# Kernel tuning notes

Measured on AMD Instinct MI355X. Metric: run time of the kernel, lower is better.

The kernel has to match this reference:

```python
import jax, jax.numpy as jnp
import numpy as np

B, L, D, H = 2, 2048, 1024, 16
DK = D // H
DFF = 4 * D
EPS = 1e-5  # torch LayerNorm default


def setup_inputs() -> dict:
    key = jax.random.key(0)
    ks = jax.random.split(key, 12)
    w = lambda k, shp: (jax.random.normal(k, shp, jnp.float32) * 0.02)
    return {
        "x": jax.random.normal(ks[0], (B, L, D), jnp.float32),
        "y": jax.random.normal(ks[1], (B, L, D), jnp.float32),
        "Wq": w(ks[2], (D, D)), "bq": jnp.zeros((D,), jnp.float32),
        "Wk": w(ks[3], (D, D)), "bk": jnp.zeros((D,), jnp.float32),
        "Wv": w(ks[4], (D, D)), "bv": jnp.zeros((D,), jnp.float32),
        "Wo": w(ks[5], (D, D)), "bo": jnp.zeros((D,), jnp.float32),
        "W1": w(ks[6], (D, DFF)), "b1": jnp.zeros((DFF,), jnp.float32),
        "W2": w(ks[7], (DFF, D)), "b2": jnp.zeros((D,), jnp.float32),
        "ln1_w": jnp.ones((L, D), jnp.float32), "ln1_b": jnp.zeros((L, D), jnp.float32),
        "ln2_w": jnp.ones((L, D), jnp.float32), "ln2_b": jnp.zeros((L, D), jnp.float32),
    }


def _layernorm2d(t, w, b):
    # nn.LayerNorm(normalized_shape=[L, D]): normalize jointly over last two dims
    mu = jnp.mean(t, axis=(-2, -1), keepdims=True)
    var = jnp.mean((t - mu) ** 2, axis=(-2, -1), keepdims=True)
    return (t - mu) * jax.lax.rsqrt(var + EPS) * w + b


def _attention(q_in, kv_in, Wq, bq, Wk, bk, Wv, bv, Wo, bo):
    split = lambda t: t.reshape(B, L, H, DK).transpose(0, 2, 1, 3)  # [B,H,L,DK]
    q = split(q_in @ Wq + bq)
    k = split(kv_in @ Wk + bk)
    v = split(kv_in @ Wv + bv)
    scores = jnp.einsum("bhqd,bhkd->bhqk", q, k) / (DK ** 0.5)
    # NOTE: original applies torch.tril to SCORES (zeroes upper triangle,
    # NOT -inf), so future positions still contribute exp(0)=1 in softmax.
    scores = jnp.tril(scores)
    p_attn = jax.nn.softmax(scores, axis=-1)
    out = jnp.einsum("bhqk,bhkd->bhqd", p_attn, v)
    out = out.transpose(0, 2, 1, 3).reshape(B, L, D)
    return out @ Wo + bo


def reference(x, y, Wq, bq, Wk, bk, Wv, bv, Wo, bo, W1, b1, W2, b2,
              ln1_w, ln1_b, ln2_w, ln2_b):
    # sublayer 0: pre-norm y, attention(query=x, key=value=norm(y)), residual
    y1 = y + _attention(x, _layernorm2d(y, ln1_w, ln1_b),
                        Wq, bq, Wk, bk, Wv, bv, Wo, bo)
    # sublayer 1: pre-norm, FFN (dropout inactive in eval), residual
    h = jax.nn.relu(_layernorm2d(y1, ln2_w, ln2_b) @ W1 + b1)
    return y1 + h @ W2 + b2
```

## Files before the change

### kernel.cpp

```cpp
#include <hip/hip_runtime.h>
#include <math.h>

#define B 2
#define L 2048
#define D 1024
#define H 16
#define DK 64
#define DFF 4096
#define EPS 1e-5f

typedef short short8 __attribute__((ext_vector_type(8)));
typedef short short4v __attribute__((ext_vector_type(4)));
typedef float float4v __attribute__((ext_vector_type(4)));
typedef unsigned int u32;

__device__ inline short f2bf(float f) {
    unsigned u = __builtin_bit_cast(unsigned, f);
    u += 0x7fffu + ((u >> 16) & 1u);
    return (short)(u >> 16);
}

__device__ inline float bf2f(short s) {
    unsigned u = ((unsigned)(unsigned short)s) << 16;
    return __builtin_bit_cast(float, u);
}

#define GLOAD_LDS16(gp, lp)                                                  \
    __builtin_amdgcn_global_load_lds(                                        \
        (const __attribute__((address_space(1))) u32*)(const void*)(gp),     \
        (__attribute__((address_space(3))) u32*)(void*)(lp), 16, 0, 0)

__device__ inline void xcd_remap(int& bx, int& by) {
    const int nbx = gridDim.x, nby = gridDim.y;
    const int orig = blockIdx.x + nbx * blockIdx.y;
    const int k = orig & 7, j = orig >> 3;
    const int nyc = nby >> 3;
    bx = j % nbx;
    by = k * nyc + j / nbx;
}


__global__ __launch_bounds__(256) void red_partial(const float* __restrict__ X,
                                                   float* __restrict__ part) {
    int b = blockIdx.y;
    const float4* p = (const float4*)(X + (size_t)b * L * D);
    float s = 0.f, ss = 0.f;
    for (int idx = blockIdx.x * 256 + threadIdx.x; idx < L * D / 4; idx += 256 * 256) {
        float4 v = p[idx];
        s += v.x + v.y + v.z + v.w;
        ss += v.x * v.x + v.y * v.y + v.z * v.z + v.w * v.w;
    }
    __shared__ float sh0[256], sh1[256];
    sh0[threadIdx.x] = s; sh1[threadIdx.x] = ss;
    __syncthreads();
    for (int o = 128; o; o >>= 1) {
        if (threadIdx.x < o) {
            sh0[threadIdx.x] += sh0[threadIdx.x + o];
            sh1[threadIdx.x] += sh1[threadIdx.x + o];
        }
        __syncthreads();
    }
    if (threadIdx.x == 0) {
        part[(b * 256 + blockIdx.x) * 2 + 0] = sh0[0];
        part[(b * 256 + blockIdx.x) * 2 + 1] = sh1[0];
    }
}

__global__ __launch_bounds__(256) void red_final(const float* __restrict__ part,
                                                 float* __restrict__ stats) {
    int b = blockIdx.x;
    float s = part[(b * 256 + threadIdx.x) * 2 + 0];
    float ss = part[(b * 256 + threadIdx.x) * 2 + 1];
    __shared__ float sh0[256], sh1[256];
    sh0[threadIdx.x] = s; sh1[threadIdx.x] = ss;
    __syncthreads();
    for (int o = 128; o; o >>= 1) {
        if (threadIdx.x < o) {
            sh0[threadIdx.x] += sh0[threadIdx.x + o];
            sh1[threadIdx.x] += sh1[threadIdx.x + o];
        }
        __syncthreads();
    }
    if (threadIdx.x == 0) {
        const float invN = 1.f / (float)(L * D);
        float mu = sh0[0] * invN;
        float var = sh1[0] * invN - mu * mu;
        stats[b * 2 + 0] = mu;
        stats[b * 2 + 1] = rsqrtf(var + EPS);
    }
}

__global__ __launch_bounds__(256) void ln_apply_bf(const float* __restrict__ X,
                                                   const float* __restrict__ W,
                                                   const float* __restrict__ Bb,
                                                   const float* __restrict__ stats,
                                                   short* __restrict__ Yn) {
    int b = blockIdx.y;
    float mu = stats[b * 2 + 0];
    float rstd = stats[b * 2 + 1];
    size_t e = (size_t)(blockIdx.x * 256 + threadIdx.x) * 4;
    const float4 xv = *(const float4*)(X + (size_t)b * L * D + e);
    const float4 wv = *(const float4*)(W + e);
    const float4 bv = *(const float4*)(Bb + e);
    short4v o;
    o[0] = f2bf((xv.x - mu) * rstd * wv.x + bv.x);
    o[1] = f2bf((xv.y - mu) * rstd * wv.y + bv.y);
    o[2] = f2bf((xv.z - mu) * rstd * wv.z + bv.z);
    o[3] = f2bf((xv.w - mu) * rstd * wv.w + bv.w);
    *(short4v*)(Yn + (size_t)b * L * D + e) = o;
}

__global__ __launch_bounds__(256) void convert_bf(const float* __restrict__ X,
                                                  short* __restrict__ Y) {
    size_t e = (size_t)(blockIdx.x * 256 + threadIdx.x) * 4;
    const float4 v = *(const float4*)(X + e);
    short4v o = {f2bf(v.x), f2bf(v.y), f2bf(v.z), f2bf(v.w)};
    *(short4v*)(Y + e) = o;
}

__global__ __launch_bounds__(256) void wt_transpose(const float* __restrict__ W,
                                                    short* __restrict__ WT,
                                                    int K, int N) {
    __shared__ short tile[32][33];
    const int t = threadIdx.x;
    const int tx = t & 31, ty = t >> 5;
    const int k0 = blockIdx.y * 32, n0 = blockIdx.x * 32;
#pragma unroll
    for (int i = 0; i < 4; ++i) {
        const int k = ty + i * 8;
        tile[k][tx] = f2bf(W[(size_t)(k0 + k) * N + n0 + tx]);
    }
    __syncthreads();
#pragma unroll
    for (int i = 0; i < 4; ++i) {
        const int n = ty + i * 8;
        WT[(size_t)(n0 + n) * K + k0 + tx] = tile[tx][n];
    }
}


__device__ __forceinline__ void cv128_body(const short* __restrict__ A,
                                           const short* __restrict__ BT,
                                           const float* __restrict__ bias,
                                           const float* __restrict__ Res,
                                           void* __restrict__ Cout,
                                           int N, int Kloop, int lda, int flags,
                                           int m0, int n0,
                                           short* __restrict__ AsB,
                                           short* __restrict__ BsB) {
    const int t = threadIdx.x;
    const int wave = t >> 6, lane = t & 63;
    const int m16 = lane & 15, q4 = lane >> 4;
    const int wm = (wave >> 1) * 64, wn = (wave & 1) * 64;
    const int xorm = m16 & 7;
    const int BUFE = 128 * 64;

    float4v acc[4][4];
#pragma unroll
    for (int i = 0; i < 4; ++i)
#pragma unroll
        for (int j = 0; j < 4; ++j) acc[i][j] = (float4v){0.f, 0.f, 0.f, 0.f};

    auto stage = [&](int buf, int k0) {
        short* AsBuf = AsB + buf * BUFE;
        short* BsBuf = BsB + buf * BUFE;
#pragma unroll
        for (int p = 0; p < 4; ++p) {
            const int s = p * 256 + t;
            const int row = s >> 3;
            const int col = ((s & 7) ^ (row & 7)) * 8;
            GLOAD_LDS16(A + (size_t)(m0 + row) * lda + k0 + col,
                        AsBuf + (p * 256 + wave * 64) * 8);
        }
#pragma unroll
        for (int p = 0; p < 4; ++p) {
            const int s = p * 256 + t;
            const int row = s >> 3;
            const int col = ((s & 7) ^ (row & 7)) * 8;
            GLOAD_LDS16(BT + (size_t)(n0 + row) * lda + k0 + col,
                        BsBuf + (p * 256 + wave * 64) * 8);
        }
    };

    auto compute = [&](int buf) {
        const short* AsBuf = AsB + buf * BUFE;
        const short* BsBuf = BsB + buf * BUFE;
#pragma unroll
        for (int kk = 0; kk < 2; ++kk) {
            const int slot = ((kk * 4 + q4) ^ xorm) * 8;
            short8 af[4], bf[4];
#pragma unroll
            for (int mi = 0; mi < 4; ++mi)
                af[mi] = *(const short8*)&AsBuf[(wm + mi * 16 + m16) * 64 + slot];
#pragma unroll
            for (int ni = 0; ni < 4; ++ni)
                bf[ni] = *(const short8*)&BsBuf[(wn + ni * 16 + m16) * 64 + slot];
#pragma unroll
            for (int mi = 0; mi < 4; ++mi)
#pragma unroll
                for (int ni = 0; ni < 4; ++ni)
                    acc[mi][ni] = __builtin_amdgcn_mfma_f32_16x16x32_bf16(
                        af[mi], bf[ni], acc[mi][ni], 0, 0, 0);
        }
    };

    const int nt = Kloop >> 6;
    stage(0, 0);
    for (int ti = 0; ti < nt; ++ti) {
        const int cur = ti & 1;
        if (ti + 1 < nt) {
            stage(cur ^ 1, (ti + 1) << 6);
            asm volatile("s_waitcnt vmcnt(8)" ::: "memory");
        } else {
            asm volatile("s_waitcnt vmcnt(0)" ::: "memory");
        }
        __builtin_amdgcn_s_barrier();
        __builtin_amdgcn_sched_barrier(0);
        compute(cur);
        __builtin_amdgcn_s_barrier();
    }

#pragma unroll
    for (int mi = 0; mi < 4; ++mi)
#pragma unroll
        for (int ni = 0; ni < 4; ++ni) {
            const int col = n0 + wn + ni * 16 + m16;
            const float bb = bias ? bias[col] : 0.f;
#pragma unroll
            for (int r = 0; r < 4; ++r) {
                const int row = m0 + wm + mi * 16 + q4 * 4 + r;
                float v = acc[mi][ni][r] + bb;
                if (Res) v += Res[(size_t)row * N + col];
                if (flags & 1) v = fmaxf(v, 0.f);
                if (flags & 2)
                    ((short*)Cout)[(size_t)row * N + col] = f2bf(v);
                else
                    ((float*)Cout)[(size_t)row * N + col] = v;
            }
        }
}

__global__ __launch_bounds__(256) void gemm_cv128(const short* __restrict__ A,
                                                  const short* __restrict__ BT,
                                                  const float* __restrict__ bias,
                                                  const float* __restrict__ Res,
                                                  void* __restrict__ Cout,
                                                  int M, int N, int K, int flags) {
    __shared__ short As[2][128 * 64];
    __shared__ short Bs[2][128 * 64];
    int bx, by;
    xcd_remap(bx, by);
    cv128_body(A, BT, bias, Res, Cout, N, K, K, flags, by * 128, bx * 128,
               &As[0][0], &Bs[0][0]);
}

__global__ __launch_bounds__(256) void gemm_qkv(const short* __restrict__ xb,
                                                const short* __restrict__ WqT,
                                                const float* __restrict__ bq,
                                                short* __restrict__ qb,
                                                const short* __restrict__ ynb,
                                                const short* __restrict__ WkvT,
                                                const float* __restrict__ bkv,
                                                short* __restrict__ kvb) {
    __shared__ short As[2][128 * 64];
    __shared__ short Bs[2][128 * 64];
    const int id = blockIdx.x;
    const int k = id & 7, j = id >> 3;
    const int lin = k * 96 + j;
    if (lin < 256) {
        const int bx = lin & 7, by = lin >> 3;
        cv128_body(xb, WqT, bq, nullptr, qb, 1024, 1024, 1024, 2,
                   by * 128, bx * 128, &As[0][0], &Bs[0][0]);
    } else {
        const int l2 = lin - 256;
        const int bx = l2 & 15, by = l2 >> 4;
        cv128_body(ynb, WkvT, bkv, nullptr, kvb, 2048, 1024, 1024, 2,
                   by * 128, bx * 128, &As[0][0], &Bs[0][0]);
    }
}

__global__ __launch_bounds__(256) void gemm_cv128_sk(const short* __restrict__ A,
                                                     const short* __restrict__ BT,
                                                     float* __restrict__ part,
                                                     int M, int N, int K) {
    __shared__ short As[2][128 * 64];
    __shared__ short Bs[2][128 * 64];
    const int id = blockIdx.x;
    const int k = id & 7, j = id >> 3;
    const int lin = k * 64 + j;
    const int ks = lin >> 8;
    const int rem = lin & 255;
    const int by = rem & 31, bx = (rem >> 5) & 7;
    const int Kc = K >> 1;
    cv128_body(A + ks * Kc, BT + ks * Kc, nullptr, nullptr,
               part + (size_t)ks * M * N, N, Kc, K, 0,
               by * 128, bx * 128, &As[0][0], &Bs[0][0]);
}

__global__ __launch_bounds__(256) void sk_reduce(const float* __restrict__ part,
                                                 const float* __restrict__ bias,
                                                 const float* __restrict__ Res,
                                                 float* __restrict__ out,
                                                 int MN, int N) {
    const size_t e = (size_t)(blockIdx.x * 256 + threadIdx.x) * 4;
    const float4 p0 = *(const float4*)(part + e);
    const float4 p1 = *(const float4*)(part + (size_t)MN + e);
    const float4 rv = *(const float4*)(Res + e);
    const float4 bv = *(const float4*)(bias + (e & (size_t)(N - 1)));
    float4 o;
    o.x = p0.x + p1.x + rv.x + bv.x;
    o.y = p0.y + p1.y + rv.y + bv.y;
    o.z = p0.z + p1.z + rv.z + bv.z;
    o.w = p0.w + p1.w + rv.w + bv.w;
    *(float4*)(out + e) = o;
}

__global__ __launch_bounds__(512) void gemm_cv256(const short* __restrict__ A,
                                                  const short* __restrict__ BT,
                                                  const float* __restrict__ bias,
                                                  const float* __restrict__ Res,
                                                  void* __restrict__ Cout,
                                                  int M, int N, int K, int flags) {
    __shared__ short As[2][256 * 64];
    __shared__ short Bs[2][256 * 64];
    const int t = threadIdx.x;
    const int wave = t >> 6, lane = t & 63;
    const int m16 = lane & 15, q4 = lane >> 4;
    int bx, by;
    xcd_remap(bx, by);
    const int m0 = by * 256, n0 = bx * 256;
    const int wm = (wave >> 2) * 128, wn = (wave & 3) * 64;
    const int xorm = m16 & 7;

    float4v acc[8][4];
#pragma unroll
    for (int i = 0; i < 8; ++i)
#pragma unroll
        for (int j = 0; j < 4; ++j) acc[i][j] = (float4v){0.f, 0.f, 0.f, 0.f};

    auto stage = [&](int buf, int k0) {
#pragma unroll
        for (int p = 0; p < 4; ++p) {
            const int s = p * 512 + t;
            const int row = s >> 3;
            const int col = ((s & 7) ^ (row & 7)) * 8;
            short* lds = &As[buf][(p * 512 + wave * 64) * 8];
            GLOAD_LDS16(A + (size_t)(m0 + row) * K + k0 + col, lds);
        }
#pragma unroll
        for (int p = 0; p < 4; ++p) {
            const int s = p * 512 + t;
            const int row = s >> 3;
            const int col = ((s & 7) ^ (row & 7)) * 8;
            short* lds = &Bs[buf][(p * 512 + wave * 64) * 8];
            GLOAD_LDS16(BT + (size_t)(n0 + row) * K + k0 + col, lds);
        }
    };

    auto compute = [&](int buf) {
#pragma unroll
        for (int kk = 0; kk < 2; ++kk) {
            const int slot = ((kk * 4 + q4) ^ xorm) * 8;
            short8 af[8], bf[4];
#pragma unroll
            for (int mi = 0; mi < 8; ++mi)
                af[mi] = *(const short8*)&As[buf][(wm + mi * 16 + m16) * 64 + slot];
#pragma unroll
            for (int ni = 0; ni < 4; ++ni)
                bf[ni] = *(const short8*)&Bs[buf][(wn + ni * 16 + m16) * 64 + slot];
#pragma unroll
            for (int mi = 0; mi < 8; ++mi)
#pragma unroll
                for (int ni = 0; ni < 4; ++ni)
                    acc[mi][ni] = __builtin_amdgcn_mfma_f32_16x16x32_bf16(
                        af[mi], bf[ni], acc[mi][ni], 0, 0, 0);
        }
    };

    const int nt = K >> 6;
    stage(0, 0);
    for (int ti = 0; ti < nt; ++ti) {
        const int cur = ti & 1;
        if (ti + 1 < nt) {
            stage(cur ^ 1, (ti + 1) << 6);
            asm volatile("s_waitcnt vmcnt(8)" ::: "memory");
        } else {
            asm volatile("s_waitcnt vmcnt(0)" ::: "memory");
        }
        __builtin_amdgcn_s_barrier();
        __builtin_amdgcn_sched_barrier(0);
        compute(cur);
        __builtin_amdgcn_s_barrier();
    }

#pragma unroll
    for (int mi = 0; mi < 8; ++mi)
#pragma unroll
        for (int ni = 0; ni < 4; ++ni) {
            const int col = n0 + wn + ni * 16 + m16;
            const float bb = bias[col];
#pragma unroll
            for (int r = 0; r < 4; ++r) {
                const int row = m0 + wm + mi * 16 + q4 * 4 + r;
                float v = acc[mi][ni][r] + bb;
                if (Res) v += Res[(size_t)row * N + col];
                if (flags & 1) v = fmaxf(v, 0.f);
                if (flags & 2)
                    ((short*)Cout)[(size_t)row * N + col] = f2bf(v);
                else
                    ((float*)Cout)[(size_t)row * N + col] = v;
            }
        }
}


#define ASTR 72
#define SKV (2 * D)

__global__ __launch_bounds__(256) void v_tilesum(const short* __restrict__ KVg,
                                                 float* __restrict__ Vtile) {
    const int bh = blockIdx.x >> 5;
    const int kt = blockIdx.x & 31;
    const int b = bh >> 4, h = bh & (H - 1);
    const size_t baseV = (size_t)b * L * SKV + (size_t)h * DK + D;
    const int d = threadIdx.x & 63, g = threadIdx.x >> 6;
    float s = 0.f;
    for (int j = g * 16; j < g * 16 + 16; ++j)
        s += bf2f(KVg[baseV + (size_t)(kt * 64 + j) * SKV + d]);
    __shared__ float sh[4][64];
    sh[g][d] = s;
    __syncthreads();
    if (threadIdx.x < 64)
        Vtile[((size_t)bh * 32 + kt) * 64 + d] = sh[0][d] + sh[1][d] + sh[2][d] + sh[3][d];
}

__global__ __launch_bounds__(64) void v_suffix(const float* __restrict__ Vtile,
                                               float* __restrict__ Vsuf) {
    const int bh = blockIdx.x;
    const int d = threadIdx.x;
    float s = 0.f;
    Vsuf[((size_t)bh * 33 + 32) * 64 + d] = 0.f;
    for (int kt = 31; kt >= 0; --kt) {
        s += Vtile[((size_t)bh * 32 + kt) * 64 + d];
        Vsuf[((size_t)bh * 33 + kt) * 64 + d] = s;
    }
}


__global__ __launch_bounds__(256) void v_transpose(const short* __restrict__ KVg,
                                                   short* __restrict__ VT) {
    __shared__ short tile[64 * ASTR];
    const int t = threadIdx.x;
    const int bh = blockIdx.x >> 5;
    const int jt = blockIdx.x & 31;
    const int b = bh >> 4, h = bh & (H - 1);
    const size_t baseV = (size_t)b * L * SKV + (size_t)h * DK + D;
    const int j0 = jt * 64;
    const int sj = t >> 3, sd8 = (t & 7) * 8, sm = t & 7;
#pragma unroll
    for (int rep = 0; rep < 2; ++rep) {
        const int j = rep * 32 + sj;
        const short8 vv = *(const short8*)(KVg + baseV + (size_t)(j0 + j) * SKV + sd8);
        const int jsw = ((((j >> 3) ^ sm) << 3) | (j & 7));
#pragma unroll
        for (int i = 0; i < 8; ++i) tile[(sd8 + i) * ASTR + jsw] = vv[i];
    }
    __syncthreads();
#pragma unroll
    for (int rep = 0; rep < 2; ++rep) {
        const int s = rep * 256 + t;
        const int d = s >> 3, c = s & 7;
        const short8 vv = *(const short8*)&tile[d * ASTR + ((c ^ (d >> 3)) << 3)];
        *(short8*)(VT + ((size_t)bh * DK + d) * L + j0 + c * 8) = vv;
    }
}


__global__ __launch_bounds__(256) void attn_mfma(const short* __restrict__ Qg,
                                                 const short* __restrict__ KVg,
                                                 const short* __restrict__ VTg,
                                                 const float* __restrict__ Vsuf,
                                                 short* __restrict__ O) {
    __shared__ alignas(16) short Kb[2][64 * 64];
    __shared__ alignas(16) short Vt[2][64 * 64];
    __shared__ alignas(16) short Pb[64 * ASTR];

    const int t = threadIdx.x;
    const int wave = t >> 6;
    const int lane = t & 63;
    const int m16 = lane & 15;
    const int q4 = lane >> 4;

    const int u = blockIdx.x & 15;
    const int bh = blockIdx.x >> 4;
    const int h = bh & (H - 1);
    const int b = bh >> 4;
    const size_t baseQ = (size_t)b * L * D + (size_t)h * DK;
    const size_t baseK = (size_t)b * L * SKV + (size_t)h * DK;
    const size_t baseVT = (size_t)bh * DK * L;

    const int irow = wave * 16 + m16;
    const int ig = irow >> 3;
    const int xorm = m16 & 7;

    auto stage = [&](int buf, int kt0) {
#pragma unroll
        for (int rep = 0; rep < 2; ++rep) {
            const int s = rep * 256 + t;
            const int j = s >> 3;
            const int c = (s & 7) ^ (j & 7);
            GLOAD_LDS16(KVg + baseK + (size_t)(kt0 + j) * SKV + c * 8,
                        &Kb[buf][(rep * 256 + wave * 64) * 8]);
        }
#pragma unroll
        for (int rep = 0; rep < 2; ++rep) {
            const int s = rep * 256 + t;
            const int d = s >> 3;
            const int c = (s & 7) ^ (d & 7);
            GLOAD_LDS16(VTg + baseVT + (size_t)d * L + kt0 + c * 8,
                        &Vt[buf][(rep * 256 + wave * 64) * 8]);
        }
    };

#pragma unroll
    for (int pq = 0; pq < 2; ++pq) {
        const int qt = pq ? (31 - u) : u;
        const int q0 = qt * 64;
        const int rowA = q0 + wave * 16 + m16;

        short8 qf[2];
#pragma unroll
        for (int kc = 0; kc < 2; ++kc)
            qf[kc] = *(const short8*)(Qg + baseQ + (size_t)rowA * D + kc * 32 + q4 * 8);

        float lsum = 0.f;
        float4v acc[4];
#pragma unroll
        for (int f = 0; f < 4; ++f) acc[f] = (float4v){0.f, 0.f, 0.f, 0.f};

        stage(0, 0);
        for (int kt = 0; kt <= qt; ++kt) {
            const int cur = kt & 1;
            if (kt < qt) {
                stage(cur ^ 1, (kt + 1) * 64);
                asm volatile("s_waitcnt vmcnt(4)" ::: "memory");
            } else {
                asm volatile("s_waitcnt vmcnt(0)" ::: "memory");
            }
            __builtin_amdgcn_s_barrier();
            __builtin_amdgcn_sched_barrier(0);

            const short* KbC = &Kb[cur][0];
            const short* VtC = &Vt[cur][0];
            const bool diag = (kt == qt);

#pragma unroll
            for (int f = 0; f < 4; ++f) {
                const int krow = f * 16 + m16;
                const short8 kf0 = *(const short8*)&KbC[krow * 64 + ((q4 ^ xorm) << 3)];
                const short8 kf1 = *(const short8*)&KbC[krow * 64 + (((4 + q4) ^ xorm) << 3)];
                float4v sv = {0.f, 0.f, 0.f, 0.f};
                sv = __builtin_amdgcn_mfma_f32_16x16x32_bf16(kf0, qf[0], sv, 0, 0, 0);
                sv = __builtin_amdgcn_mfma_f32_16x16x32_bf16(kf1, qf[1], sv, 0, 0, 0);

                float pv[4];
                if (diag) {
#pragma unroll
                    for (int r = 0; r < 4; ++r) {
                        const int jl = f * 16 + q4 * 4 + r;
                        pv[r] = (jl <= irow) ? __expf(sv[r] * 0.125f) : 1.0f;
                    }
                } else {
#pragma unroll
                    for (int r = 0; r < 4; ++r) pv[r] = __expf(sv[r] * 0.125f);
                }
                lsum += pv[0] + pv[1] + pv[2] + pv[3];

                short4v s4;
                s4[0] = f2bf(pv[0]); s4[1] = f2bf(pv[1]);
                s4[2] = f2bf(pv[2]); s4[3] = f2bf(pv[3]);
                const int jb = f * 2 + (q4 >> 1);
                *(short4v*)&Pb[irow * ASTR + (((jb ^ ig) << 3) | ((q4 & 1) << 2))] = s4;
            }

#pragma unroll
            for (int kc = 0; kc < 2; ++kc) {
                const short8 pf = *(const short8*)&Pb[irow * ASTR + (((kc * 4 + q4) ^ ig) << 3)];
#pragma unroll
                for (int f = 0; f < 4; ++f) {
                    const int d = f * 16 + m16;
                    const short8 vf = *(const short8*)&VtC[d * 64 + (((kc * 4 + q4) ^ xorm) << 3)];
                    acc[f] = __builtin_amdgcn_mfma_f32_16x16x32_bf16(pf, vf, acc[f], 0, 0, 0);
                }
            }
            __builtin_amdgcn_s_barrier();
        }

        float s = lsum;
        s += __shfl_xor(s, 16);
        s += __shfl_xor(s, 32);
        s += (float)(L - (qt + 1) * 64);
        const float inv = 1.0f / s;
        float invr[4];
#pragma unroll
        for (int r = 0; r < 4; ++r) invr[r] = __shfl(inv, q4 * 4 + r);

        const float* vs = Vsuf + ((size_t)bh * 33 + qt + 1) * 64;
#pragma unroll
        for (int f = 0; f < 4; ++f) {
            const float vadd = vs[f * 16 + m16];
#pragma unroll
            for (int r = 0; r < 4; ++r) {
                const int i = q0 + wave * 16 + q4 * 4 + r;
                O[baseQ + (size_t)i * D + f * 16 + m16] = f2bf((acc[f][r] + vadd) * invr[r]);
            }
        }
    }
}


extern "C" void kernel_launch(void* const* d_in, const int* in_sizes, int n_in,
                              void* d_out, int out_size, void* d_ws, size_t ws_size,
                              hipStream_t stream) {
    const float* x    = (const float*)d_in[0];
    const float* y    = (const float*)d_in[1];
    const float* Wq   = (const float*)d_in[2];
    const float* bq   = (const float*)d_in[3];
    const float* Wk   = (const float*)d_in[4];
    const float* bk   = (const float*)d_in[5];
    const float* Wv   = (const float*)d_in[6];
    const float* bv   = (const float*)d_in[7];
    const float* Wo   = (const float*)d_in[8];
    const float* bo   = (const float*)d_in[9];
    const float* W1   = (const float*)d_in[10];
    const float* b1   = (const float*)d_in[11];
    const float* W2   = (const float*)d_in[12];
    const float* b2   = (const float*)d_in[13];
    const float* ln1w = (const float*)d_in[14];
    const float* ln1b = (const float*)d_in[15];
    const float* ln2w = (const float*)d_in[16];
    const float* ln2b = (const float*)d_in[17];
    float* out = (float*)d_out;

    const size_t F = (size_t)B * L * D;
    char* p = (char*)d_ws;
    short* xb    = (short*)p; p += F * 2;
    short* ynb   = (short*)p; p += F * 2;
    short* qb    = (short*)p; p += F * 2;
    short* kvb   = (short*)p; p += 2 * F * 2;
    short* aob   = (short*)p; p += F * 2;
    short* y1nb  = (short*)p; p += F * 2;
    short* hb    = (short*)p; p += (size_t)B * L * DFF * 2;
    float* y1    = (float*)p; p += F * 4;
    short* WqT   = (short*)p; p += (size_t)D * D * 2;
    short* WkvT  = (short*)p; p += (size_t)D * 2 * D * 2;
    short* WoT   = (short*)p; p += (size_t)D * D * 2;
    short* W1T   = (short*)p; p += (size_t)D * DFF * 2;
    short* W2T   = (short*)p; p += (size_t)D * DFF * 2;
    float* biaskv= (float*)p; p += 2 * D * 4;
    float* vtile = (float*)p; p += (size_t)B * H * 32 * DK * 4;
    float* vsuf  = (float*)p; p += (size_t)B * H * 33 * DK * 4;
    float* part  = (float*)p; p += B * 256 * 2 * 4;
    float* stats = (float*)p;

    short* vtb = hb;
    float* skpart = (float*)qb;

    const int M = B * L;

    wt_transpose<<<dim3(D / 32, D / 32), 256, 0, stream>>>(Wq, WqT, D, D);
    wt_transpose<<<dim3(D / 32, D / 32), 256, 0, stream>>>(Wk, WkvT, D, D);
    wt_transpose<<<dim3(D / 32, D / 32), 256, 0, stream>>>(Wv, WkvT + (size_t)D * D, D, D);
    wt_transpose<<<dim3(D / 32, D / 32), 256, 0, stream>>>(Wo, WoT, D, D);
    wt_transpose<<<dim3(DFF / 32, D / 32), 256, 0, stream>>>(W1, W1T, D, DFF);
    wt_transpose<<<dim3(D / 32, DFF / 32), 256, 0, stream>>>(W2, W2T, DFF, D);
    hipMemcpyAsync(biaskv,     bk, D * sizeof(float), hipMemcpyDeviceToDevice, stream);
    hipMemcpyAsync(biaskv + D, bv, D * sizeof(float), hipMemcpyDeviceToDevice, stream);

    convert_bf<<<dim3(F / 1024), 256, 0, stream>>>(x, xb);

    red_partial<<<dim3(256, B), 256, 0, stream>>>(y, part);
    red_final<<<dim3(B), 256, 0, stream>>>(part, stats);
    ln_apply_bf<<<dim3(L * D / 1024, B), 256, 0, stream>>>(y, ln1w, ln1b, stats, ynb);

    gemm_qkv<<<dim3(768), 256, 0, stream>>>(xb, WqT, bq, qb, ynb, WkvT, biaskv, kvb);

    v_transpose<<<dim3(B * H * 32), 256, 0, stream>>>(kvb, vtb);
    v_tilesum<<<dim3(B * H * 32), 256, 0, stream>>>(kvb, vtile);
    v_suffix<<<dim3(B * H), 64, 0, stream>>>(vtile, vsuf);

    attn_mfma<<<dim3(B * H * 16), 256, 0, stream>>>(qb, kvb, vtb, vsuf, aob);

    gemm_cv128<<<dim3(D / 128, M / 128), 256, 0, stream>>>(aob, WoT, bo, y, y1, M, D, D, 0);

    red_partial<<<dim3(256, B), 256, 0, stream>>>(y1, part);
    red_final<<<dim3(B), 256, 0, stream>>>(part, stats);
    ln_apply_bf<<<dim3(L * D / 1024, B), 256, 0, stream>>>(y1, ln2w, ln2b, stats, y1nb);

    gemm_cv256<<<dim3(DFF / 256, M / 256), 512, 0, stream>>>(y1nb, W1T, b1, nullptr, hb, M, DFF, D, 3);

    gemm_cv128_sk<<<dim3(512), 256, 0, stream>>>(hb, W2T, skpart, M, D, DFF);
    sk_reduce<<<dim3(M * D / 1024), 256, 0, stream>>>(skpart, b2, y1, out, M * D, D);
}
```

Baseline: 429.3 us.

## Merge weight transposes, fuse V tilesum, triple-buffer attention, split-K Wo GEMM

Folds the six weight-transpose launches into one kernel and fuses the V tile-sum into the V transpose kernel, which cuts launch count and an extra read of V. The attention kernel moves to a three-stage K/V buffer, raises wave priority around the MFMA section, uses exp2f with a folded scale, and packs the bf16 conversion with v_cvt_pk_bf16_f32. The Wo projection switches from a 128x128 tiled GEMM to the split-K GEMM plus a reduction kernel. The extra buffer stage uses more LDS, which can lower occupancy, and split-K adds an extra pass over partial sums.

Result: faster. 410.6 us (-4.3%).

```diff
diff --git a/kernel.cpp b/kernel.cpp
--- a/kernel.cpp
+++ b/kernel.cpp
@@ -118,13 +118,28 @@
     *(short4v*)(Y + e) = o;
 }
 
-__global__ __launch_bounds__(256) void wt_transpose(const float* __restrict__ W,
-                                                    short* __restrict__ WT,
-                                                    int K, int N) {
+__global__ __launch_bounds__(256) void wt_transpose_all(
+        const float* __restrict__ Wq, const float* __restrict__ Wk,
+        const float* __restrict__ Wv, const float* __restrict__ Wo,
+        const float* __restrict__ W1, const float* __restrict__ W2,
+        short* __restrict__ WqT, short* __restrict__ WkvT,
+        short* __restrict__ WoT, short* __restrict__ W1T,
+        short* __restrict__ W2T) {
+    const int id = blockIdx.x;
+    const float* W; short* WT; int K, N, rel;
+    if (id < 1024)      { W = Wq; WT = WqT;                    K = 1024; N = 1024; rel = id; }
+    else if (id < 2048) { W = Wk; WT = WkvT;                   K = 1024; N = 1024; rel = id - 1024; }
+    else if (id < 3072) { W = Wv; WT = WkvT + (size_t)D * D;   K = 1024; N = 1024; rel = id - 2048; }
+    else if (id < 4096) { W = Wo; WT = WoT;                    K = 1024; N = 1024; rel = id - 3072; }
+    else if (id < 8192) { W = W1; WT = W1T;                    K = 1024; N = 4096; rel = id - 4096; }
+    else                { W = W2; WT = W2T;                    K = 4096; N = 1024; rel = id - 8192; }
+    const int lb = (N == 4096) ? 7 : 5;
+    const int bx = rel & ((1 << lb) - 1), by = rel >> lb;
+
     __shared__ short tile[32][33];
     const int t = threadIdx.x;
     const int tx = t & 31, ty = t >> 5;
-    const int k0 = blockIdx.y * 32, n0 = blockIdx.x * 32;
+    const int k0 = by * 32, n0 = bx * 32;
 #pragma unroll
     for (int i = 0; i < 4; ++i) {
         const int k = ty + i * 8;
@@ -238,20 +253,6 @@
                     ((float*)Cout)[(size_t)row * N + col] = v;
             }
         }
-}
-
-__global__ __launch_bounds__(256) void gemm_cv128(const short* __restrict__ A,
-                                                  const short* __restrict__ BT,
-                                                  const float* __restrict__ bias,
-                                                  const float* __restrict__ Res,
-                                                  void* __restrict__ Cout,
-                                                  int M, int N, int K, int flags) {
-    __shared__ short As[2][128 * 64];
-    __shared__ short Bs[2][128 * 64];
-    int bx, by;
-    xcd_remap(bx, by);
-    cv128_body(A, BT, bias, Res, Cout, N, K, K, flags, by * 128, bx * 128,
-               &As[0][0], &Bs[0][0]);
 }
 
 __global__ __launch_bounds__(256) void gemm_qkv(const short* __restrict__ xb,
@@ -417,21 +418,45 @@
 #define ASTR 72
 #define SKV (2 * D)
 
-__global__ __launch_bounds__(256) void v_tilesum(const short* __restrict__ KVg,
-                                                 float* __restrict__ Vtile) {
+__global__ __launch_bounds__(256) void v_transpose(const short* __restrict__ KVg,
+                                                   short* __restrict__ VT,
+                                                   float* __restrict__ Vtile) {
+    __shared__ short tile[64 * ASTR];
+    __shared__ float sh[4][64];
+    const int t = threadIdx.x;
     const int bh = blockIdx.x >> 5;
-    const int kt = blockIdx.x & 31;
+    const int jt = blockIdx.x & 31;
     const int b = bh >> 4, h = bh & (H - 1);
     const size_t baseV = (size_t)b * L * SKV + (size_t)h * DK + D;
-    const int d = threadIdx.x & 63, g = threadIdx.x >> 6;
-    float s = 0.f;
-    for (int j = g * 16; j < g * 16 + 16; ++j)
-        s += bf2f(KVg[baseV + (size_t)(kt * 64 + j) * SKV + d]);
-    __shared__ float sh[4][64];
-    sh[g][d] = s;
+    const int j0 = jt * 64;
+    const int sj = t >> 3, sd8 = (t & 7) * 8, sm = t & 7;
+#pragma unroll
+    for (int rep = 0; rep < 2; ++rep) {
+        const int j = rep * 32 + sj;
+        const short8 vv = *(const short8*)(KVg + baseV + (size_t)(j0 + j) * SKV + sd8);
+        const int jsw = ((((j >> 3) ^ sm) << 3) | (j & 7));
+#pragma unroll
+        for (int i = 0; i < 8; ++i) tile[(sd8 + i) * ASTR + jsw] = vv[i];
+    }
     __syncthreads();
-    if (threadIdx.x < 64)
-        Vtile[((size_t)bh * 32 + kt) * 64 + d] = sh[0][d] + sh[1][d] + sh[2][d] + sh[3][d];
+#pragma unroll
+    for (int rep = 0; rep < 2; ++rep) {
+        const int s = rep * 256 + t;
+        const int d = s >> 3, c = s & 7;
+        const short8 vv = *(const short8*)&tile[d * ASTR + ((c ^ (d >> 3)) << 3)];
+        *(short8*)(VT + ((size_t)bh * DK + d) * L + j0 + c * 8) = vv;
+    }
+    {
+        const int d = t & 63, g = t >> 6;
+        float s = 0.f;
+#pragma unroll
+        for (int c = 0; c < 16; ++c) s += bf2f(tile[d * ASTR + g * 16 + c]);
+        sh[g][d] = s;
+        __syncthreads();
+        if (t < 64)
+            Vtile[((size_t)bh * 32 + jt) * 64 + t] =
+                sh[0][t] + sh[1][t] + sh[2][t] + sh[3][t];
+    }
 }
 
 __global__ __launch_bounds__(64) void v_suffix(const float* __restrict__ Vtile,
@@ -447,42 +472,13 @@
 }
 
 
-__global__ __launch_bounds__(256) void v_transpose(const short* __restrict__ KVg,
-                                                   short* __restrict__ VT) {
-    __shared__ short tile[64 * ASTR];
-    const int t = threadIdx.x;
-    const int bh = blockIdx.x >> 5;
-    const int jt = blockIdx.x & 31;
-    const int b = bh >> 4, h = bh & (H - 1);
-    const size_t baseV = (size_t)b * L * SKV + (size_t)h * DK + D;
-    const int j0 = jt * 64;
-    const int sj = t >> 3, sd8 = (t & 7) * 8, sm = t & 7;
-#pragma unroll
-    for (int rep = 0; rep < 2; ++rep) {
-        const int j = rep * 32 + sj;
-        const short8 vv = *(const short8*)(KVg + baseV + (size_t)(j0 + j) * SKV + sd8);
-        const int jsw = ((((j >> 3) ^ sm) << 3) | (j & 7));
-#pragma unroll
-        for (int i = 0; i < 8; ++i) tile[(sd8 + i) * ASTR + jsw] = vv[i];
-    }
-    __syncthreads();
-#pragma unroll
-    for (int rep = 0; rep < 2; ++rep) {
-        const int s = rep * 256 + t;
-        const int d = s >> 3, c = s & 7;
-        const short8 vv = *(const short8*)&tile[d * ASTR + ((c ^ (d >> 3)) << 3)];
-        *(short8*)(VT + ((size_t)bh * DK + d) * L + j0 + c * 8) = vv;
-    }
-}
-
-
 __global__ __launch_bounds__(256) void attn_mfma(const short* __restrict__ Qg,
                                                  const short* __restrict__ KVg,
                                                  const short* __restrict__ VTg,
                                                  const float* __restrict__ Vsuf,
                                                  short* __restrict__ O) {
-    __shared__ alignas(16) short Kb[2][64 * 64];
-    __shared__ alignas(16) short Vt[2][64 * 64];
+    __shared__ alignas(16) short Kb[3][64 * 64];
+    __shared__ alignas(16) short Vt[3][64 * 64];
     __shared__ alignas(16) short Pb[64 * ASTR];
 
     const int t = threadIdx.x;
@@ -539,10 +535,13 @@
         for (int f = 0; f < 4; ++f) acc[f] = (float4v){0.f, 0.f, 0.f, 0.f};
 
         stage(0, 0);
+        if (qt >= 1) stage(1, 64);
         for (int kt = 0; kt <= qt; ++kt) {
-            const int cur = kt & 1;
-            if (kt < qt) {
-                stage(cur ^ 1, (kt + 1) * 64);
+            const int cur = kt % 3;
+            if (kt + 2 <= qt) {
+                stage((kt + 2) % 3, (kt + 2) * 64);
+                asm volatile("s_waitcnt vmcnt(8)" ::: "memory");
+            } else if (kt + 1 <= qt) {
                 asm volatile("s_waitcnt vmcnt(4)" ::: "memory");
             } else {
                 asm volatile("s_waitcnt vmcnt(0)" ::: "memory");
@@ -554,6 +553,7 @@
             const short* VtC = &Vt[cur][0];
             const bool diag = (kt == qt);
 
+            __builtin_amdgcn_s_setprio(1);
 #pragma unroll
             for (int f = 0; f < 4; ++f) {
                 const int krow = f * 16 + m16;
@@ -568,19 +568,21 @@
 #pragma unroll
                     for (int r = 0; r < 4; ++r) {
                         const int jl = f * 16 + q4 * 4 + r;
-                        pv[r] = (jl <= irow) ? __expf(sv[r] * 0.125f) : 1.0f;
+                        pv[r] = (jl <= irow) ? exp2f(sv[r] * 0.18033688f) : 1.0f;
                     }
                 } else {
 #pragma unroll
-                    for (int r = 0; r < 4; ++r) pv[r] = __expf(sv[r] * 0.125f);
+                    for (int r = 0; r < 4; ++r) pv[r] = exp2f(sv[r] * 0.18033688f);
                 }
                 lsum += pv[0] + pv[1] + pv[2] + pv[3];
 
-                short4v s4;
-                s4[0] = f2bf(pv[0]); s4[1] = f2bf(pv[1]);
-                s4[2] = f2bf(pv[2]); s4[3] = f2bf(pv[3]);
+                u32 r0, r1;
+                asm("v_cvt_pk_bf16_f32 %0, %1, %2" : "=v"(r0) : "v"(pv[0]), "v"(pv[1]));
+                asm("v_cvt_pk_bf16_f32 %0, %1, %2" : "=v"(r1) : "v"(pv[2]), "v"(pv[3]));
                 const int jb = f * 2 + (q4 >> 1);
-                *(short4v*)&Pb[irow * ASTR + (((jb ^ ig) << 3) | ((q4 & 1) << 2))] = s4;
+                u32* pdst = (u32*)&Pb[irow * ASTR + (((jb ^ ig) << 3) | ((q4 & 1) << 2))];
+                pdst[0] = r0;
+                pdst[1] = r1;
             }
 
 #pragma unroll
@@ -593,6 +595,7 @@
                     acc[f] = __builtin_amdgcn_mfma_f32_16x16x32_bf16(pf, vf, acc[f], 0, 0, 0);
                 }
             }
+            __builtin_amdgcn_s_setprio(0);
             __builtin_amdgcn_s_barrier();
         }
 
@@ -664,16 +667,13 @@
     float* stats = (float*)p;
 
     short* vtb = hb;
+    float* skpartWo = (float*)hb;
     float* skpart = (float*)qb;
 
     const int M = B * L;
 
-    wt_transpose<<<dim3(D / 32, D / 32), 256, 0, stream>>>(Wq, WqT, D, D);
-    wt_transpose<<<dim3(D / 32, D / 32), 256, 0, stream>>>(Wk, WkvT, D, D);
-    wt_transpose<<<dim3(D / 32, D / 32), 256, 0, stream>>>(Wv, WkvT + (size_t)D * D, D, D);
-    wt_transpose<<<dim3(D / 32, D / 32), 256, 0, stream>>>(Wo, WoT, D, D);
-    wt_transpose<<<dim3(DFF / 32, D / 32), 256, 0, stream>>>(W1, W1T, D, DFF);
-    wt_transpose<<<dim3(D / 32, DFF / 32), 256, 0, stream>>>(W2, W2T, DFF, D);
+    wt_transpose_all<<<dim3(12288), 256, 0, stream>>>(Wq, Wk, Wv, Wo, W1, W2,
+                                                      WqT, WkvT, WoT, W1T, W2T);
     hipMemcpyAsync(biaskv,     bk, D * sizeof(float), hipMemcpyDeviceToDevice, stream);
     hipMemcpyAsync(biaskv + D, bv, D * sizeof(float), hipMemcpyDeviceToDevice, stream);
 
@@ -685,13 +685,13 @@
 
     gemm_qkv<<<dim3(768), 256, 0, stream>>>(xb, WqT, bq, qb, ynb, WkvT, biaskv, kvb);
 
-    v_transpose<<<dim3(B * H * 32), 256, 0, stream>>>(kvb, vtb);
-    v_tilesum<<<dim3(B * H * 32), 256, 0, stream>>>(kvb, vtile);
+    v_transpose<<<dim3(B * H * 32), 256, 0, stream>>>(kvb, vtb, vtile);
     v_suffix<<<dim3(B * H), 64, 0, stream>>>(vtile, vsuf);
 
     attn_mfma<<<dim3(B * H * 16), 256, 0, stream>>>(qb, kvb, vtb, vsuf, aob);
 
-    gemm_cv128<<<dim3(D / 128, M / 128), 256, 0, stream>>>(aob, WoT, bo, y, y1, M, D, D, 0);
+    gemm_cv128_sk<<<dim3(512), 256, 0, stream>>>(aob, WoT, skpartWo, M, D, D);
+    sk_reduce<<<dim3(M * D / 1024), 256, 0, stream>>>(skpartWo, bo, y, y1, M * D, D);
 
     red_partial<<<dim3(256, B), 256, 0, stream>>>(y1, part);
     red_final<<<dim3(B), 256, 0, stream>>>(part, stats);
```
